# Kernel tuning notes

Measured on AMD Instinct MI355X. Metric: run time of the kernel, lower is better.

## Reference

```python
import jax, jax.numpy as jnp
import numpy as np

B, S, E = 8, 2048, 1024
DROPOUT_P = 0.1


def setup_inputs() -> dict:
    key = jax.random.key(0)
    kq, kk, kv, km, kw, kb = jax.random.split(key, 6)
    query = jax.random.normal(kq, (B, S, E), dtype=jnp.float32)
    key_t = jax.random.normal(kk, (B, S, E), dtype=jnp.float32)
    value = jax.random.normal(kv, (B, S, E), dtype=jnp.float32)
    # inverted dropout mask: keep with prob 1-p, scale kept by 1/(1-p)
    keep = jax.random.bernoulli(km, 1.0 - DROPOUT_P, (B, S, S))
    dropout_mask = keep.astype(jnp.float32) / (1.0 - DROPOUT_P)
    Wout = jax.random.normal(kw, (E, E), dtype=jnp.float32) * (E ** -0.5)
    bout = jax.random.normal(kb, (E,), dtype=jnp.float32) * 0.01
    return {
        "query": query,
        "key": key_t,
        "value": value,
        "dropout_mask": dropout_mask,
        "Wout": Wout,
        "bout": bout,
        "inv_scale_factor": 32,  # sqrt(E) = sqrt(1024)
    }


def reference(query, key, value, dropout_mask, Wout, bout, inv_scale_factor):
    # scores: [B, S, S]
    scores = jnp.einsum("bqd,bkd->bqk", query, key) / jnp.float32(inv_scale_factor)
    probs = jax.nn.softmax(scores, axis=-1)
    probs = probs * dropout_mask  # inverted dropout
    attn = jnp.einsum("bqk,bkd->bqd", probs, value)  # [B, S, E]
    # fc_out: torch Linear -> x @ W.T + b
    return jnp.einsum("bqd,ed->bqe", attn, Wout) + bout
```

## Files before the change

kernel.cpp:

```cpp
#include <hip/hip_runtime.h>
#include <cstdint>
#include <cstddef>

typedef short short8 __attribute__((ext_vector_type(8)));
typedef float f32x4 __attribute__((ext_vector_type(4)));

static __device__ __forceinline__ ushort f2bf(float f) {
  union { float f; uint32_t u; } v; v.f = f;
  uint32_t u = v.u + 0x7fffu + ((v.u >> 16) & 1u);
  return (ushort)(u >> 16);
}

static __device__ __forceinline__ void g2lds16(const ushort* g, ushort* lds) {
  __builtin_amdgcn_global_load_lds(
      (const __attribute__((address_space(1))) void*)(uintptr_t)g,
      (__attribute__((address_space(3))) void*)(uintptr_t)lds,
      16, 0, 0);
}

#define VMW(n) asm volatile("s_waitcnt vmcnt(" #n ")" ::: "memory")
#define BAR()  asm volatile("s_barrier" ::: "memory")

__global__ __launch_bounds__(256) void convert_qk_bf16(
    const float* __restrict__ Q, const float* __restrict__ K,
    ushort* __restrict__ Qb, ushort* __restrict__ Kb) {
  const bool second = blockIdx.x >= 8192;
  const float* src = second ? K : Q;
  ushort* dst = second ? Kb : Qb;
  const size_t i = ((size_t)(blockIdx.x & 8191) * 256 + threadIdx.x) * 8;
  const float4 a = *(const float4*)(src + i);
  const float4 b = *(const float4*)(src + i + 4);
  ushort4 o0, o1;
  o0.x = f2bf(a.x); o0.y = f2bf(a.y); o0.z = f2bf(a.z); o0.w = f2bf(a.w);
  o1.x = f2bf(b.x); o1.y = f2bf(b.y); o1.z = f2bf(b.z); o1.w = f2bf(b.w);
  *(ushort4*)(dst + i) = o0;
  *(ushort4*)(dst + i + 4) = o1;
}

__global__ __launch_bounds__(256) void convert_w_bf16(
    const float* __restrict__ W, ushort* __restrict__ Wb) {
  const size_t i = ((size_t)blockIdx.x * 256 + threadIdx.x) * 8;
  const float4 a = *(const float4*)(W + i);
  const float4 b = *(const float4*)(W + i + 4);
  ushort4 o0, o1;
  o0.x = f2bf(a.x); o0.y = f2bf(a.y); o0.z = f2bf(a.z); o0.w = f2bf(a.w);
  o1.x = f2bf(b.x); o1.y = f2bf(b.y); o1.z = f2bf(b.z); o1.w = f2bf(b.w);
  *(ushort4*)(Wb + i) = o0;
  *(ushort4*)(Wb + i + 4) = o1;
}

__global__ __launch_bounds__(256) void transpose_convert_v(
    const float* __restrict__ V, ushort* __restrict__ Vt) {
  __shared__ float t[64][65];
  const int b = blockIdx.z;
  const int d0 = blockIdx.x * 64;
  const int k0 = blockIdx.y * 64;
  const float* Vb = V + (size_t)b * 2048 * 1024;
  ushort* Vtb = Vt + (size_t)b * 1024 * 2048;
  const int tx = threadIdx.x & 63, ty = threadIdx.x >> 6;
#pragma unroll
  for (int j = 0; j < 64; j += 4)
    t[ty + j][tx] = Vb[(size_t)(k0 + ty + j) * 1024 + d0 + tx];
  __syncthreads();
  const int lk = (threadIdx.x & 31) * 2;
  const int ld = threadIdx.x >> 5;
#pragma unroll
  for (int p = 0; p < 8; ++p) {
    const int d = ld + p * 8;
    const uint32_t val =
        (uint32_t)f2bf(t[lk][d]) | ((uint32_t)f2bf(t[lk + 1][d]) << 16);
    *(uint32_t*)&Vtb[(size_t)(d0 + d) * 2048 + k0 + lk] = val;
  }
}

template <int EPI>
__global__ __launch_bounds__(512, 2) void gemm256(
    const ushort* __restrict__ Ap, const ushort* __restrict__ Bp,
    void* __restrict__ Cp, int M, int N, int K,
    size_t sA, size_t sB, size_t sC, float scale,
    const float* __restrict__ bias, const float* __restrict__ mask,
    float* __restrict__ rowsum) {
  constexpr int BK = 32;
  __shared__ __align__(16) ushort As[4][256 * BK];
  __shared__ __align__(16) ushort Bs[4][256 * BK];
  const int tid = threadIdx.x;

  const int gx = gridDim.x, gy = gridDim.y;
  const int nwg = gx * gy * gridDim.z;
  int li = blockIdx.x + gx * (blockIdx.y + gy * blockIdx.z);
  li = (li & 7) * (nwg >> 3) + (li >> 3);
  const int bn = li % gx;
  const int rst = li / gx;
  const int bm = rst % gy;
  const int z = rst / gy;

  const int lane = tid & 63, w = tid >> 6;
  const int quad = lane >> 4, l16 = lane & 15;
  const int wm = w >> 2, wn = w & 3;
  const int NT = K >> 5;

  f32x4 acc[8][4];
#pragma unroll
  for (int i = 0; i < 8; ++i)
#pragma unroll
    for (int j = 0; j < 4; ++j) acc[i][j] = (f32x4){0.f, 0.f, 0.f, 0.f};

  const int srow = w * 16 + (lane >> 2);
  const int sgran = (lane & 3) ^ ((lane >> 3) & 3);
  const ushort* Abase = Ap + sA * z + (size_t)bm * 256 * K;
  const ushort* Bbase = Bp + sB * z + (size_t)bn * 256 * K;
  const ushort* Ag0 = Abase + (size_t)srow * K + sgran * 8;
  const ushort* Ag1 = Ag0 + (size_t)128 * K;
  const ushort* Bg0 = Bbase + (size_t)srow * K + sgran * 8;
  const ushort* Bg1 = Bg0 + (size_t)128 * K;
  const int ldsw0 = (w * 16) * BK;
  const int ldsw1 = (128 + w * 16) * BK;

  auto STAGE_A = [&](int t) {
    ushort* a = As[t & 3];
    const size_t ko = (size_t)t * BK;
    g2lds16(Ag0 + ko, a + ldsw0);
    g2lds16(Ag1 + ko, a + ldsw1);
  };
  auto STAGE_B = [&](int t) {
    ushort* b = Bs[t & 3];
    const size_t ko = (size_t)t * BK;
    g2lds16(Bg0 + ko, b + ldsw0);
    g2lds16(Bg1 + ko, b + ldsw1);
  };

  const int pg = quad ^ ((l16 >> 1) & 3);
  const int aoff = (wm * 128 + l16) * BK + pg * 8;
  const int boff = (wn * 64 + l16) * BK + pg * 8;

  auto TILE = [&](int t, bool stage_ok) {
    const ushort* a = As[t & 3];
    const ushort* b = Bs[t & 3];
    short8 bfv[4], af[4];
#pragma unroll
    for (int tn = 0; tn < 4; ++tn)
      bfv[tn] = *(const short8*)&b[boff + tn * 16 * BK];
#pragma unroll
    for (int tm = 0; tm < 4; ++tm)
      af[tm] = *(const short8*)&a[aoff + tm * 16 * BK];
    if (stage_ok) STAGE_A(t + 3);
    BAR();
    __builtin_amdgcn_s_setprio(1);
#pragma unroll
    for (int tm = 0; tm < 4; ++tm)
#pragma unroll
      for (int tn = 0; tn < 4; ++tn)
        acc[tm][tn] = __builtin_amdgcn_mfma_f32_16x16x32_bf16(
            af[tm], bfv[tn], acc[tm][tn], 0, 0, 0);
    __builtin_amdgcn_s_setprio(0);
    BAR();
    short8 af2[4];
#pragma unroll
    for (int tm = 0; tm < 4; ++tm)
      af2[tm] = *(const short8*)&a[aoff + (4 + tm) * 16 * BK];
    if (stage_ok) STAGE_B(t + 3);
    BAR();
    __builtin_amdgcn_s_setprio(1);
#pragma unroll
    for (int tm = 0; tm < 4; ++tm)
#pragma unroll
      for (int tn = 0; tn < 4; ++tn)
        acc[4 + tm][tn] = __builtin_amdgcn_mfma_f32_16x16x32_bf16(
            af2[tm], bfv[tn], acc[4 + tm][tn], 0, 0, 0);
    __builtin_amdgcn_s_setprio(0);
  };

  STAGE_A(0); STAGE_B(0);
  STAGE_A(1); STAGE_B(1);
  STAGE_A(2); STAGE_B(2);
  for (int t = 0; t < NT - 2; ++t) {
    VMW(8);
    BAR();
    TILE(t, t + 3 < NT);
  }
  VMW(4);
  BAR();
  TILE(NT - 2, false);
  VMW(0);
  BAR();
  TILE(NT - 1, false);

  const size_t cz = sC * z;
  if constexpr (EPI == 1) {
    ushort* Cb = (ushort*)Cp + cz;
    const float* Mb = mask + (size_t)z * 2048 * 2048;
    float rs[8][4];
#pragma unroll
    for (int tm = 0; tm < 8; ++tm)
#pragma unroll
      for (int r = 0; r < 4; ++r) rs[tm][r] = 0.f;
#pragma unroll
    for (int tm = 0; tm < 8; ++tm) {
      const int grb = bm * 256 + wm * 128 + tm * 16 + quad * 4;
#pragma unroll
      for (int r = 0; r < 4; ++r) {
        const size_t rowoff = (size_t)(grb + r) * N;
        const float* mrow = Mb + rowoff;
        ushort* crow = Cb + rowoff;
#pragma unroll
        for (int tn = 0; tn < 4; ++tn) {
          const int gc = bn * 256 + wn * 64 + tn * 16 + l16;
          const float e = __expf(acc[tm][tn][r] * scale);
          rs[tm][r] += e;
          crow[gc] = f2bf(e * mrow[gc]);
        }
      }
    }
#pragma unroll
    for (int tm = 0; tm < 8; ++tm)
#pragma unroll
      for (int r = 0; r < 4; ++r) {
        float v = rs[tm][r];
        v += __shfl_xor(v, 1);
        v += __shfl_xor(v, 2);
        v += __shfl_xor(v, 4);
        v += __shfl_xor(v, 8);
        if (l16 == ((tm * 4 + r) & 15))
          atomicAdd(&rowsum[(size_t)z * 2048 + bm * 256 + wm * 128 + tm * 16 +
                            quad * 4 + r],
                    v);
      }
  } else if constexpr (EPI == 2) {
    ushort* Cb = (ushort*)Cp + cz;
#pragma unroll
    for (int tm = 0; tm < 8; ++tm) {
      const int grb = bm * 256 + wm * 128 + tm * 16 + quad * 4;
#pragma unroll
      for (int r = 0; r < 4; ++r) {
        const float linv = 1.0f / rowsum[(size_t)z * 2048 + grb + r];
#pragma unroll
        for (int tn = 0; tn < 4; ++tn) {
          const int gc = bn * 256 + wn * 64 + tn * 16 + l16;
          Cb[(size_t)(grb + r) * N + gc] = f2bf(acc[tm][tn][r] * linv);
        }
      }
    }
  } else {
    float* Cb = (float*)Cp + cz;
#pragma unroll
    for (int tn = 0; tn < 4; ++tn) {
      const int gc = bn * 256 + wn * 64 + tn * 16 + l16;
      const float bv = bias[gc];
#pragma unroll
      for (int tm = 0; tm < 8; ++tm) {
        const int grb = bm * 256 + wm * 128 + tm * 16 + quad * 4;
#pragma unroll
        for (int r = 0; r < 4; ++r)
          Cb[(size_t)(grb + r) * N + gc] = acc[tm][tn][r] * scale + bv;
      }
    }
  }
}

extern "C" void kernel_launch(void* const* d_in, const int* in_sizes, int n_in,
                              void* d_out, int out_size, void* d_ws,
                              size_t ws_size, hipStream_t stream) {
  (void)in_sizes; (void)n_in; (void)out_size; (void)ws_size;
  const float* Q    = (const float*)d_in[0];
  const float* Kmat = (const float*)d_in[1];
  const float* V    = (const float*)d_in[2];
  const float* mask = (const float*)d_in[3];
  const float* W    = (const float*)d_in[4];
  const float* bout = (const float*)d_in[5];
  float* out = (float*)d_out;

  ushort* RegA = (ushort*)d_ws;
  ushort* RegB = RegA + (size_t)16 * 1024 * 1024;
  ushort* P    = RegB + (size_t)16 * 1024 * 1024;
  float* rowsum = out;

  hipMemsetAsync(rowsum, 0, (size_t)8 * 2048 * sizeof(float), stream);
  convert_qk_bf16<<<dim3(16384), 256, 0, stream>>>(Q, Kmat, RegA, RegB);
  gemm256<1><<<dim3(8, 8, 8), 512, 0, stream>>>(
      RegA, RegB, P, 2048, 2048, 1024,
      (size_t)2048 * 1024, (size_t)2048 * 1024, (size_t)2048 * 2048,
      1.0f / 32.0f, nullptr, mask, rowsum);
  transpose_convert_v<<<dim3(16, 32, 8), 256, 0, stream>>>(V, RegA);
  gemm256<2><<<dim3(4, 8, 8), 512, 0, stream>>>(
      P, RegA, RegB, 2048, 1024, 2048,
      (size_t)2048 * 2048, (size_t)1024 * 2048, (size_t)2048 * 1024,
      1.0f, nullptr, nullptr, rowsum);
  convert_w_bf16<<<dim3(512), 256, 0, stream>>>(W, RegA);
  gemm256<0><<<dim3(4, 64, 1), 512, 0, stream>>>(
      RegB, RegA, out, 16384, 1024, 1024, 0, 0, 0, 1.0f, bout, nullptr,
      nullptr);
}
```

Baseline: 532.9 us.

## Stage GEMM epilogue through LDS for coalesced vectorized row stores

The epilogue now writes the accumulator tile into a swizzled region of LDS that reuses the staging buffers. It does this for one 128-row half at a time, then reads it back so each wave owns full rows. Mask loads and C stores become 16-byte vectors spanning contiguous 256-column rows instead of scattered 2-byte and 4-byte accesses. Row-sum reduction now takes one atomic per row per wave. The cost is extra barriers, LDS traffic, and half the waves idling during each phase.

```diff
diff --git a/kernel.cpp b/kernel.cpp
--- a/kernel.cpp
+++ b/kernel.cpp
@@ -81,8 +81,7 @@
     const float* __restrict__ bias, const float* __restrict__ mask,
     float* __restrict__ rowsum) {
   constexpr int BK = 32;
-  __shared__ __align__(16) ushort As[4][256 * BK];
-  __shared__ __align__(16) ushort Bs[4][256 * BK];
+  __shared__ __align__(16) ushort smem[2][4][256 * BK];
   const int tid = threadIdx.x;
 
   const int gx = gridDim.x, gy = gridDim.y;
@@ -117,13 +116,13 @@
   const int ldsw1 = (128 + w * 16) * BK;
 
   auto STAGE_A = [&](int t) {
-    ushort* a = As[t & 3];
+    ushort* a = &smem[0][t & 3][0];
     const size_t ko = (size_t)t * BK;
     g2lds16(Ag0 + ko, a + ldsw0);
     g2lds16(Ag1 + ko, a + ldsw1);
   };
   auto STAGE_B = [&](int t) {
-    ushort* b = Bs[t & 3];
+    ushort* b = &smem[1][t & 3][0];
     const size_t ko = (size_t)t * BK;
     g2lds16(Bg0 + ko, b + ldsw0);
     g2lds16(Bg1 + ko, b + ldsw1);
@@ -134,8 +133,8 @@
   const int boff = (wn * 64 + l16) * BK + pg * 8;
 
   auto TILE = [&](int t, bool stage_ok) {
-    const ushort* a = As[t & 3];
-    const ushort* b = Bs[t & 3];
+    const ushort* a = &smem[0][t & 3][0];
+    const ushort* b = &smem[1][t & 3][0];
     short8 bfv[4], af[4];
 #pragma unroll
     for (int tn = 0; tn < 4; ++tn)
@@ -185,73 +184,65 @@
   BAR();
   TILE(NT - 1, false);
 
+  float* S = (float*)&smem[0][0][0];
   const size_t cz = sC * z;
-  if constexpr (EPI == 1) {
-    ushort* Cb = (ushort*)Cp + cz;
-    const float* Mb = mask + (size_t)z * 2048 * 2048;
-    float rs[8][4];
-#pragma unroll
-    for (int tm = 0; tm < 8; ++tm)
-#pragma unroll
-      for (int r = 0; r < 4; ++r) rs[tm][r] = 0.f;
-#pragma unroll
-    for (int tm = 0; tm < 8; ++tm) {
-      const int grb = bm * 256 + wm * 128 + tm * 16 + quad * 4;
-#pragma unroll
-      for (int r = 0; r < 4; ++r) {
-        const size_t rowoff = (size_t)(grb + r) * N;
-        const float* mrow = Mb + rowoff;
-        ushort* crow = Cb + rowoff;
-#pragma unroll
-        for (int tn = 0; tn < 4; ++tn) {
-          const int gc = bn * 256 + wn * 64 + tn * 16 + l16;
-          const float e = __expf(acc[tm][tn][r] * scale);
-          rs[tm][r] += e;
-          crow[gc] = f2bf(e * mrow[gc]);
+  float4 bv4;
+  if constexpr (EPI == 0) bv4 = *(const float4*)&bias[bn * 256 + lane * 4];
+
+  for (int h = 0; h < 2; ++h) {
+    BAR();
+    if (wm == h) {
+#pragma unroll
+      for (int tm = 0; tm < 8; ++tm)
+#pragma unroll
+        for (int r = 0; r < 4; ++r) {
+          const int rloc = tm * 16 + quad * 4 + r;
+#pragma unroll
+          for (int tn = 0; tn < 4; ++tn) {
+            const int pgw = (wn * 4 + tn) ^ quad;
+            S[rloc * 256 + pgw * 16 + l16] = acc[tm][tn][r];
+          }
         }
-      }
     }
-#pragma unroll
-    for (int tm = 0; tm < 8; ++tm)
-#pragma unroll
-      for (int r = 0; r < 4; ++r) {
-        float v = rs[tm][r];
-        v += __shfl_xor(v, 1);
-        v += __shfl_xor(v, 2);
-        v += __shfl_xor(v, 4);
-        v += __shfl_xor(v, 8);
-        if (l16 == ((tm * 4 + r) & 15))
-          atomicAdd(&rowsum[(size_t)z * 2048 + bm * 256 + wm * 128 + tm * 16 +
-                            quad * 4 + r],
-                    v);
-      }
-  } else if constexpr (EPI == 2) {
-    ushort* Cb = (ushort*)Cp + cz;
-#pragma unroll
-    for (int tm = 0; tm < 8; ++tm) {
-      const int grb = bm * 256 + wm * 128 + tm * 16 + quad * 4;
-#pragma unroll
-      for (int r = 0; r < 4; ++r) {
-        const float linv = 1.0f / rowsum[(size_t)z * 2048 + grb + r];
-#pragma unroll
-        for (int tn = 0; tn < 4; ++tn) {
-          const int gc = bn * 256 + wn * 64 + tn * 16 + l16;
-          Cb[(size_t)(grb + r) * N + gc] = f2bf(acc[tm][tn][r] * linv);
+    BAR();
+    if (wm == h) {
+#pragma unroll
+      for (int i = 0; i < 32; ++i) {
+        const int rloc = wn * 32 + i;
+        const int swz = (i >> 2) & 3;
+        const f32x4 v = *(const f32x4*)&S[rloc * 256 +
+                                          (((lane >> 2) ^ swz) << 4) +
+                                          ((lane & 3) << 2)];
+        const int grow = bm * 256 + h * 128 + rloc;
+        const int gcol = bn * 256 + lane * 4;
+        const size_t ro = (size_t)grow * N + gcol;
+        if constexpr (EPI == 1) {
+          const float e0 = __expf(v[0] * scale), e1 = __expf(v[1] * scale),
+                      e2 = __expf(v[2] * scale), e3 = __expf(v[3] * scale);
+          float part = (e0 + e1) + (e2 + e3);
+          const float4 mv =
+              *(const float4*)(mask + (size_t)z * 2048 * 2048 + ro);
+          ushort4 o;
+          o.x = f2bf(e0 * mv.x); o.y = f2bf(e1 * mv.y);
+          o.z = f2bf(e2 * mv.z); o.w = f2bf(e3 * mv.w);
+          *(ushort4*)((ushort*)Cp + cz + ro) = o;
+#pragma unroll
+          for (int off = 32; off >= 1; off >>= 1)
+            part += __shfl_xor(part, off);
+          if (lane == 0)
+            atomicAdd(&rowsum[(size_t)z * 2048 + grow], part);
+        } else if constexpr (EPI == 2) {
+          const float linv = 1.0f / rowsum[(size_t)z * 2048 + grow];
+          ushort4 o;
+          o.x = f2bf(v[0] * linv); o.y = f2bf(v[1] * linv);
+          o.z = f2bf(v[2] * linv); o.w = f2bf(v[3] * linv);
+          *(ushort4*)((ushort*)Cp + cz + ro) = o;
+        } else {
+          float4 o;
+          o.x = v[0] * scale + bv4.x; o.y = v[1] * scale + bv4.y;
+          o.z = v[2] * scale + bv4.z; o.w = v[3] * scale + bv4.w;
+          *(float4*)((float*)Cp + cz + ro) = o;
         }
-      }
-    }
-  } else {
-    float* Cb = (float*)Cp + cz;
-#pragma unroll
-    for (int tn = 0; tn < 4; ++tn) {
-      const int gc = bn * 256 + wn * 64 + tn * 16 + l16;
-      const float bv = bias[gc];
-#pragma unroll
-      for (int tm = 0; tm < 8; ++tm) {
-        const int grb = bm * 256 + wm * 128 + tm * 16 + quad * 4;
-#pragma unroll
-        for (int r = 0; r < 4; ++r)
-          Cb[(size_t)(grb + r) * N + gc] = acc[tm][tn][r] * scale + bv;
       }
     }
   }
```

Result: slower. 663.7 us (+24.5%).
